# Optimization experiments

Hardware: AMD Instinct MI355X
Metric: run time of the kernel (lower is better)

## Reference

```python
import jax, jax.numpy as jnp
import numpy as np

B, T, C, H = 2, 4096, 768, 12
D = C // H  # head_dim = 64


def setup_inputs() -> dict:
    key = jax.random.key(0)
    k1, k2, k3 = jax.random.split(key, 3)
    x = jax.random.normal(k1, (B, T, C), dtype=jnp.float32)
    w_qkv = jax.random.normal(k2, (C, 3 * C), dtype=jnp.float32) * (1.0 / np.sqrt(C))
    w_out = jax.random.normal(k3, (C, C), dtype=jnp.float32) * (1.0 / np.sqrt(C))
    return {"x": x, "w_qkv": w_qkv, "w_out": w_out}


def reference(x, w_qkv, w_out):
    b, t, c = x.shape
    qkv = x @ w_qkv                              # (B,T,3C)
    q, k, v = jnp.split(qkv, 3, axis=-1)
    # (B,T,C) -> (B,H,T,D)
    q = q.reshape(b, t, H, D).transpose(0, 2, 1, 3)
    k = k.reshape(b, t, H, D).transpose(0, 2, 1, 3)
    v = v.reshape(b, t, H, D).transpose(0, 2, 1, 3)
    att = jnp.einsum('bhqd,bhkd->bhqk', q, k) / jnp.sqrt(jnp.float32(D))
    causal = jnp.tril(jnp.ones((t, t), dtype=bool))  # True where allowed
    att = jnp.where(causal, att, -jnp.inf)
    att = jax.nn.softmax(att, axis=-1)
    y = jnp.einsum('bhqk,bhkd->bhqd', att, v)        # (B,H,T,D)
    y = y.transpose(0, 2, 1, 3).reshape(b, t, c)
    return y @ w_out
```

## Files before the change

kernel.cpp:

```cpp
#include <hip/hip_runtime.h>
#include <stdint.h>
#include <stddef.h>

#define NB 2
#define NT 4096
#define NC 768
#define NH 12
#define ND 64

typedef unsigned short u16;
typedef __attribute__((ext_vector_type(4))) float f32x4;
typedef __attribute__((ext_vector_type(16))) float f32x16;
typedef __attribute__((ext_vector_type(8))) unsigned short u16x8;
typedef __attribute__((ext_vector_type(4))) unsigned short u16x4;
typedef __attribute__((ext_vector_type(8))) __bf16 bf16x8;
typedef __attribute__((ext_vector_type(4))) unsigned int u32x4;

__device__ __forceinline__ u16 f2bf(float f) {
  uint32_t u = __builtin_bit_cast(uint32_t, f);
  u += 0x7FFFu + ((u >> 16) & 1u);
  return (u16)(u >> 16);
}
__device__ __forceinline__ bf16x8 asbf(u16x8 v) { return __builtin_bit_cast(bf16x8, v); }

__device__ __forceinline__ uint32_t pkbf(float a, float b) {
  uint32_t ua = __builtin_bit_cast(uint32_t, a) + 0x8000u;
  uint32_t ub = __builtin_bit_cast(uint32_t, b) + 0x8000u;
  return __builtin_amdgcn_perm(ub, ua, 0x07060302u);
}
__device__ __forceinline__ uint32_t pktr(float a, float b) {
  return __builtin_amdgcn_perm(__builtin_bit_cast(uint32_t, b),
                               __builtin_bit_cast(uint32_t, a), 0x07060302u);
}

__global__ void k_cast(const float* __restrict__ in, u16* __restrict__ out, int n4) {
  int i = blockIdx.x * blockDim.x + threadIdx.x;
  if (i < n4) {
    f32x4 v = ((const f32x4*)in)[i];
    u16x4 o;
    o[0] = f2bf(v[0]); o[1] = f2bf(v[1]); o[2] = f2bf(v[2]); o[3] = f2bf(v[3]);
    ((u16x4*)out)[i] = o;
  }
}

__global__ void k_transpose(const float* __restrict__ in, u16* __restrict__ out,
                            int R, int Cn) {
  __shared__ float tile[32][33];
  int c0 = blockIdx.x * 32, r0 = blockIdx.y * 32;
  int tx = threadIdx.x & 31, ty = threadIdx.x >> 5;
  for (int i = ty; i < 32; i += 8)
    tile[i][tx] = in[(size_t)(r0 + i) * Cn + c0 + tx];
  __syncthreads();
  for (int i = ty; i < 32; i += 8)
    out[(size_t)(c0 + i) * R + r0 + tx] = f2bf(tile[tx][i]);
}

template <int EPI>
__global__ __launch_bounds__(256, 2)
void k_gemm_bt(const u16* __restrict__ A, const u16* __restrict__ Bt,
               int M, int N, int K,
               u16* __restrict__ o0, u16* __restrict__ o1, u16* __restrict__ o2,
               float* __restrict__ of) {
  __shared__ u16 As[128 * 40];
  __shared__ u16 Bs[128 * 40];
  const int tid = threadIdx.x;
  const int wave = tid >> 6, lane = tid & 63, quad = lane >> 4, lc = lane & 15;
  const int wm = (wave & 1) * 64, wn = (wave >> 1) * 64;
  const int bm = blockIdx.y * 128, bn = blockIdx.x * 128;

  const int sr = tid >> 2;
  const int sc8 = (tid & 3) * 8;
  const u16* ap0 = A + (size_t)(bm + sr) * K + sc8;
  const u16* ap1 = A + (size_t)(bm + 64 + sr) * K + sc8;
  const u16* bp0 = Bt + (size_t)(bn + sr) * K + sc8;
  const u16* bp1 = Bt + (size_t)(bn + 64 + sr) * K + sc8;
  u16* asl0 = &As[sr * 40 + sc8];
  u16* asl1 = &As[(64 + sr) * 40 + sc8];
  u16* bsl0 = &Bs[sr * 40 + sc8];
  u16* bsl1 = &Bs[(64 + sr) * 40 + sc8];

  f32x4 zv = {0.f, 0.f, 0.f, 0.f};
  f32x4 acc[4][4];
#pragma unroll
  for (int i = 0; i < 4; ++i)
#pragma unroll
    for (int j = 0; j < 4; ++j) acc[i][j] = zv;

  for (int k0 = 0; k0 < K; k0 += 32) {
    u16x8 a0 = *(const u16x8*)(ap0 + k0);
    u16x8 a1 = *(const u16x8*)(ap1 + k0);
    u16x8 b0 = *(const u16x8*)(bp0 + k0);
    u16x8 b1 = *(const u16x8*)(bp1 + k0);
    __syncthreads();
    *(u16x8*)asl0 = a0;
    *(u16x8*)asl1 = a1;
    *(u16x8*)bsl0 = b0;
    *(u16x8*)bsl1 = b1;
    __syncthreads();

    bf16x8 af[4], bfv[4];
#pragma unroll
    for (int mi = 0; mi < 4; ++mi)
      af[mi] = asbf(*(const u16x8*)&As[(wm + mi * 16 + lc) * 40 + quad * 8]);
#pragma unroll
    for (int ni = 0; ni < 4; ++ni)
      bfv[ni] = asbf(*(const u16x8*)&Bs[(wn + ni * 16 + lc) * 40 + quad * 8]);
#pragma unroll
    for (int mi = 0; mi < 4; ++mi)
#pragma unroll
      for (int ni = 0; ni < 4; ++ni)
        acc[mi][ni] = __builtin_amdgcn_mfma_f32_16x16x32_bf16(af[mi], bfv[ni],
                                                              acc[mi][ni], 0, 0, 0);
  }

  const int mrow0 = bm + wm + quad * 4;
#pragma unroll
  for (int mi = 0; mi < 4; ++mi) {
    const int mbase = mrow0 + mi * 16;
#pragma unroll
    for (int ni = 0; ni < 4; ++ni) {
      const int n = bn + wn + ni * 16 + lc;
      if (EPI == 0) {
#pragma unroll
        for (int r = 0; r < 4; ++r)
          of[(size_t)(mbase + r) * N + n] = acc[mi][ni][r];
      } else {
        const int sect = n / NC;
        const int wn2 = n - sect * NC;
        const int h = wn2 >> 6, d = wn2 & 63;
        const int b = mbase >> 12;
        const int t = mbase & (NT - 1);
        const float sc = (sect == 0) ? 0.18033688011112042f : 1.0f;
        if (sect == 2) {
          u16x4 pk;
#pragma unroll
          for (int r = 0; r < 4; ++r) pk[r] = f2bf(acc[mi][ni][r]);
          *(u16x4*)&o2[((size_t)(b * NH + h) * ND + d) * NT + t] = pk;
        } else {
          u16* dst = (sect == 0) ? o0 : o1;
#pragma unroll
          for (int r = 0; r < 4; ++r)
            dst[((size_t)(b * NH + h) * NT + (t + r)) * ND + d] =
                f2bf(acc[mi][ni][r] * sc);
        }
      }
    }
  }
}

__device__ __forceinline__ void softpack16(const f32x16& s, int qrel, bool msk,
                                           int l5, float& sl, bf16x8* pf) {
  float e[16];
#pragma unroll
  for (int r = 0; r < 16; ++r) {
    float v = s[r];
    if (msk) {
      int tl = (r & 3) + 8 * (r >> 2) + 4 * l5;
      v = (tl > qrel) ? -1e30f : v;
    }
    e[r] = exp2f(v);
    sl += __builtin_bit_cast(float,
          __builtin_bit_cast(uint32_t, e[r]) & 0xFFFF0000u);
  }
  uint32_t wv[8];
#pragma unroll
  for (int i = 0; i < 8; ++i) wv[i] = pktr(e[2 * i], e[2 * i + 1]);
#pragma unroll
  for (int g = 0; g < 2; ++g) {
    auto r0 = __builtin_amdgcn_permlane32_swap(wv[g * 4 + 0], wv[g * 4 + 2], false, false);
    auto r1 = __builtin_amdgcn_permlane32_swap(wv[g * 4 + 1], wv[g * 4 + 3], false, false);
    u32x4 f = {r0[0], r1[0], r0[1], r1[1]};
    pf[g] = __builtin_bit_cast(bf16x8, f);
  }
}

__global__ __launch_bounds__(256, 3)
void k_attn(const u16* __restrict__ Q, const u16* __restrict__ K,
            const u16* __restrict__ Vt, u16* __restrict__ Y) {
  __shared__ u16 SM[2][64 * 64];
  __shared__ float PL[2][64];
  const int tid = threadIdx.x;
  const int lane = tid & 63, wave = tid >> 6;
  const int l5 = lane >> 5, l31 = lane & 31;
  const int qh = wave & 1, th = wave >> 1;
  const int bh = blockIdx.x % (NB * NH);
  const int qi = 63 - blockIdx.x / (NB * NH);
  const int b = bh / NH, h = bh - b * NH;
  const u16* __restrict__ Qb = Q + (size_t)bh * NT * ND;
  const u16* __restrict__ Kb = K + (size_t)bh * NT * ND;
  const u16* __restrict__ Vb = Vt + (size_t)bh * (size_t)ND * NT;

  const int qg = qi * 64 + qh * 32 + l31;

  bf16x8 bq[4];
#pragma unroll
  for (int ks = 0; ks < 4; ++ks)
    bq[ks] = asbf(*(const u16x8*)(Qb + (size_t)qg * ND + ks * 16 + l5 * 8));

  f32x16 Zv;
#pragma unroll
  for (int i = 0; i < 16; ++i) Zv[i] = 0.f;
  f32x16 o0 = Zv, o1 = Zv;
  float sl = 0.f;

  const int srow = tid >> 3, sg = tid & 7;
  const int soff = srow * 64 + ((sg ^ (srow & 7)) * 8);
  const u16* __restrict__ pK = Kb + (size_t)srow * ND + sg * 8;
  const u16* __restrict__ pV = Vb + (size_t)srow * NT + sg * 8;

  int qfro[4];
#pragma unroll
  for (int ks = 0; ks < 4; ++ks)
    qfro[ks] = (th * 32 + l31) * 64 + (((ks * 2 + l5) ^ (l31 & 7)) * 8);
  int vfro[2];
#pragma unroll
  for (int kp = 0; kp < 2; ++kp)
    vfro[kp] = l31 * 64 + ((((2 * th + kp) * 2 + l5) ^ (l31 & 7)) * 8);

  u16x8 st[4];
  st[0] = *(const u16x8*)(pK);
  st[1] = *(const u16x8*)(pK + (size_t)32 * ND);
  st[2] = *(const u16x8*)(pV);
  st[3] = *(const u16x8*)(pV + (size_t)32 * NT);

#pragma unroll 1
  for (int tau = 0; tau <= qi; ++tau) {
    __syncthreads();
    *(u16x8*)&SM[0][soff] = st[0];
    *(u16x8*)&SM[0][2048 + soff] = st[1];
    *(u16x8*)&SM[1][soff] = st[2];
    *(u16x8*)&SM[1][2048 + soff] = st[3];
    __syncthreads();

    const bool dg = (tau == qi);
    const bool act = !(dg && th > qh);
    bf16x8 p[2];
    if (act) {
      f32x16 s = Zv;
#pragma unroll
      for (int ks = 0; ks < 4; ++ks) {
        bf16x8 kf = asbf(*(const u16x8*)&SM[0][qfro[ks]]);
        s = __builtin_amdgcn_mfma_f32_32x32x16_bf16(kf, bq[ks], s, 0, 0, 0);
      }
      softpack16(s, l31, dg && (th == qh), l5, sl, p);
    }

    if (tau < qi) {
      const int tn = (tau + 1) * 64;
      st[0] = *(const u16x8*)(pK + (size_t)tn * ND);
      st[1] = *(const u16x8*)(pK + (size_t)(tn + 32) * ND);
      st[2] = *(const u16x8*)(pV + tn);
      st[3] = *(const u16x8*)(pV + (size_t)32 * NT + tn);
    }

    if (act) {
#pragma unroll
      for (int kp = 0; kp < 2; ++kp) {
        bf16x8 v0 = asbf(*(const u16x8*)&SM[1][vfro[kp]]);
        bf16x8 v1 = asbf(*(const u16x8*)&SM[1][2048 + vfro[kp]]);
        o0 = __builtin_amdgcn_mfma_f32_32x32x16_bf16(v0, p[kp], o0, 0, 0, 0);
        o1 = __builtin_amdgcn_mfma_f32_32x32x16_bf16(v1, p[kp], o1, 0, 0, 0);
      }
    }
  }

  float l = sl + __shfl_xor(sl, 32);
  __syncthreads();
  float* PK = (float*)&SM[0][0];
  if (th == 0) {
#pragma unroll
    for (int r = 0; r < 16; ++r) PK[(qh * 32 + r) * 64 + lane] = o0[r];
#pragma unroll
    for (int r = 0; r < 16; ++r) PK[(qh * 32 + 16 + r) * 64 + lane] = o1[r];
    PL[qh][lane] = l;
  }
  __syncthreads();
  if (th == 1) {
#pragma unroll
    for (int r = 0; r < 16; ++r) o0[r] += PK[(qh * 32 + r) * 64 + lane];
#pragma unroll
    for (int r = 0; r < 16; ++r) o1[r] += PK[(qh * 32 + 16 + r) * 64 + lane];
    l += PL[qh][lane];
    const float inv = 1.f / l;
    u16* yrow = Y + (size_t)(b * NT + qg) * NC + h * 64;
#pragma unroll
    for (int dh = 0; dh < 2; ++dh) {
      const f32x16& o = dh ? o1 : o0;
#pragma unroll
      for (int rq = 0; rq < 4; ++rq) {
        const int d = dh * 32 + 8 * rq + 4 * l5;
        uint2 w;
        w.x = pkbf(o[rq * 4 + 0] * inv, o[rq * 4 + 1] * inv);
        w.y = pkbf(o[rq * 4 + 2] * inv, o[rq * 4 + 3] * inv);
        *(uint2*)&yrow[d] = w;
      }
    }
  }
}

extern "C" void kernel_launch(void* const* d_in, const int* in_sizes, int n_in,
                              void* d_out, int out_size, void* d_ws, size_t ws_size,
                              hipStream_t stream) {
  (void)in_sizes; (void)n_in; (void)out_size; (void)ws_size;
  const float* x = (const float*)d_in[0];
  const float* w_qkv = (const float*)d_in[1];
  const float* w_out = (const float*)d_in[2];
  float* out = (float*)d_out;

  u16* ws = (u16*)d_ws;
  const size_t XE = (size_t)NB * NT * NC;
  u16* xb  = ws;
  u16* wqT = xb + XE;
  u16* woT = wqT + (size_t)3 * NC * NC;
  u16* Qb  = woT + (size_t)NC * NC;
  u16* Kb  = Qb + XE;
  u16* Vtb = Kb + XE;
  u16* yb  = Vtb + XE;

  k_cast<<<(int)(XE / 4 / 256), 256, 0, stream>>>(x, xb, (int)(XE / 4));
  k_transpose<<<dim3(3 * NC / 32, NC / 32), 256, 0, stream>>>(w_qkv, wqT, NC, 3 * NC);
  k_transpose<<<dim3(NC / 32, NC / 32), 256, 0, stream>>>(w_out, woT, NC, NC);
  k_gemm_bt<1><<<dim3(3 * NC / 128, NB * NT / 128), 256, 0, stream>>>(
      xb, wqT, NB * NT, 3 * NC, NC, Qb, Kb, Vtb, nullptr);
  k_attn<<<dim3((NB * NH) * 64), 256, 0, stream>>>(Qb, Kb, Vtb, yb);
  k_gemm_bt<0><<<dim3(NC / 128, NB * NT / 128), 256, 0, stream>>>(
      yb, woT, NB * NT, NC, NC, nullptr, nullptr, nullptr, out);
}
```

Before: 246.8 us.

## Double query tile per block, double-buffer K/V via direct global-to-LDS loads

The attention kernel now handles a 128-query tile per block, so each wave holds two 32-row query fragments that share every loaded K/V tile. K and V are streamed into double-buffered LDS with global_load_lds, replacing the register staging and the two syncthreads per step with waitcnt and raw barriers. Blocks are remapped with a permuted tile order to balance causal work, and the diagonal masking is specialised through a template. This cuts LDS staging traffic and barrier count per FLOP, at the cost of more accumulator registers and more LDS per block, which could lower occupancy.

```diff
diff --git a/kernel.cpp b/kernel.cpp
--- a/kernel.cpp
+++ b/kernel.cpp
@@ -15,6 +15,9 @@
 typedef __attribute__((ext_vector_type(4))) unsigned short u16x4;
 typedef __attribute__((ext_vector_type(8))) __bf16 bf16x8;
 typedef __attribute__((ext_vector_type(4))) unsigned int u32x4;
+
+typedef __attribute__((address_space(1))) const unsigned int gu32;
+typedef __attribute__((address_space(3))) unsigned int lu32;
 
 __device__ __forceinline__ u16 f2bf(float f) {
   uint32_t u = __builtin_bit_cast(uint32_t, f);
@@ -148,15 +151,17 @@
   }
 }
 
-__device__ __forceinline__ void softpack16(const f32x16& s, int qrel, bool msk,
-                                           int l5, float& sl, bf16x8* pf) {
+
+template <bool MSK>
+__device__ __forceinline__ void softpackT(const f32x16& s, int l31, int l5,
+                                          float& sl, bf16x8* pf) {
   float e[16];
 #pragma unroll
   for (int r = 0; r < 16; ++r) {
     float v = s[r];
-    if (msk) {
+    if (MSK) {
       int tl = (r & 3) + 8 * (r >> 2) + 4 * l5;
-      v = (tl > qrel) ? -1e30f : v;
+      v = (tl > l31) ? -1e30f : v;
     }
     e[r] = exp2f(v);
     sl += __builtin_bit_cast(float,
@@ -174,39 +179,54 @@
   }
 }
 
+#define GLDS(gsrc, ldst) __builtin_amdgcn_global_load_lds( \
+    (gu32*)(gsrc), (lu32*)(ldst), 16, 0, 0)
+
 __global__ __launch_bounds__(256, 3)
 void k_attn(const u16* __restrict__ Q, const u16* __restrict__ K,
             const u16* __restrict__ Vt, u16* __restrict__ Y) {
-  __shared__ u16 SM[2][64 * 64];
-  __shared__ float PL[2][64];
+  __shared__ u16 RAW[2 * 8192 + 768];
+  __shared__ float PLs[128];
   const int tid = threadIdx.x;
   const int lane = tid & 63, wave = tid >> 6;
   const int l5 = lane >> 5, l31 = lane & 31;
   const int qh = wave & 1, th = wave >> 1;
-  const int bh = blockIdx.x % (NB * NH);
-  const int qi = 63 - blockIdx.x / (NB * NH);
+  const int o_ = blockIdx.x;
+  const int bh = o_ >> 5;
+  const int jj = ((((o_ & 31) + bh) & 31) * 11) & 31;
   const int b = bh / NH, h = bh - b * NH;
   const u16* __restrict__ Qb = Q + (size_t)bh * NT * ND;
   const u16* __restrict__ Kb = K + (size_t)bh * NT * ND;
   const u16* __restrict__ Vb = Vt + (size_t)bh * (size_t)ND * NT;
 
-  const int qg = qi * 64 + qh * 32 + l31;
-
-  bf16x8 bq[4];
-#pragma unroll
-  for (int ks = 0; ks < 4; ++ks)
-    bq[ks] = asbf(*(const u16x8*)(Qb + (size_t)qg * ND + ks * 16 + l5 * 8));
+  const int Qb0 = jj * 128;
+  const int qu0 = 4 * jj + 2 * qh;
+  const int ntau = 2 * jj + 2;
+
+  const int qgA = Qb0 + qh * 64 + l31;
+  const int qgB = qgA + 32;
+  bf16x8 bqA[4], bqB[4];
+#pragma unroll
+  for (int ks = 0; ks < 4; ++ks) {
+    bqA[ks] = asbf(*(const u16x8*)(Qb + (size_t)qgA * ND + ks * 16 + l5 * 8));
+    bqB[ks] = asbf(*(const u16x8*)(Qb + (size_t)qgB * ND + ks * 16 + l5 * 8));
+  }
 
   f32x16 Zv;
 #pragma unroll
   for (int i = 0; i < 16; ++i) Zv[i] = 0.f;
-  f32x16 o0 = Zv, o1 = Zv;
-  float sl = 0.f;
-
-  const int srow = tid >> 3, sg = tid & 7;
-  const int soff = srow * 64 + ((sg ^ (srow & 7)) * 8);
-  const u16* __restrict__ pK = Kb + (size_t)srow * ND + sg * 8;
-  const u16* __restrict__ pV = Vb + (size_t)srow * NT + sg * 8;
+  f32x16 oA0 = Zv, oA1 = Zv, oB0 = Zv, oB1 = Zv;
+  float slA = 0.f, slB = 0.f;
+
+  const int lr = lane >> 3;
+  const int gsw = ((lane & 7) ^ lr) * 8;
+  const int r0w = wave * 16;
+  const u16* gk0 = Kb + (size_t)(r0w + lr) * ND + gsw;
+  const u16* gk1 = gk0 + (size_t)8 * ND;
+  const u16* gv0 = Vb + (size_t)(r0w + lr) * NT + gsw;
+  const u16* gv1 = gv0 + (size_t)8 * NT;
+  u16* lk0 = &RAW[r0w * 64];
+  u16* lv0 = &RAW[4096 + r0w * 64];
 
   int qfro[4];
 #pragma unroll
@@ -215,84 +235,113 @@
   int vfro[2];
 #pragma unroll
   for (int kp = 0; kp < 2; ++kp)
-    vfro[kp] = l31 * 64 + ((((2 * th + kp) * 2 + l5) ^ (l31 & 7)) * 8);
-
-  u16x8 st[4];
-  st[0] = *(const u16x8*)(pK);
-  st[1] = *(const u16x8*)(pK + (size_t)32 * ND);
-  st[2] = *(const u16x8*)(pV);
-  st[3] = *(const u16x8*)(pV + (size_t)32 * NT);
+    vfro[kp] = 4096 + l31 * 64 + (((4 * th + 2 * kp + l5) ^ (l31 & 7)) * 8);
+
+  GLDS(gk0, lk0);
+  GLDS(gk1, lk0 + 512);
+  GLDS(gv0, lv0);
+  GLDS(gv1, lv0 + 512);
 
 #pragma unroll 1
-  for (int tau = 0; tau <= qi; ++tau) {
-    __syncthreads();
-    *(u16x8*)&SM[0][soff] = st[0];
-    *(u16x8*)&SM[0][2048 + soff] = st[1];
-    *(u16x8*)&SM[1][soff] = st[2];
-    *(u16x8*)&SM[1][2048 + soff] = st[3];
-    __syncthreads();
-
-    const bool dg = (tau == qi);
-    const bool act = !(dg && th > qh);
-    bf16x8 p[2];
-    if (act) {
-      f32x16 s = Zv;
+  for (int tau = 0; tau < ntau; ++tau) {
+    const int p = tau & 1;
+    if (tau + 1 < ntau) {
+      const int tn = (tau + 1) * 64;
+      const int bo = (p ^ 1) * 8192;
+      GLDS(gk0 + (size_t)tn * ND, lk0 + bo);
+      GLDS(gk1 + (size_t)tn * ND, lk0 + bo + 512);
+      GLDS(gv0 + tn, lv0 + bo);
+      GLDS(gv1 + tn, lv0 + bo + 512);
+      asm volatile("s_waitcnt vmcnt(4)" ::: "memory");
+    } else {
+      asm volatile("s_waitcnt vmcnt(0)" ::: "memory");
+    }
+    __builtin_amdgcn_s_barrier();
+
+    const int u = 2 * tau + th;
+    const int d0 = qu0 - u;
+    if (d0 >= -1) {
+      const bool act0 = (d0 >= 0);
+      const u16* bufp = &RAW[p * 8192];
+
+      f32x16 sA = Zv, sB = Zv;
 #pragma unroll
       for (int ks = 0; ks < 4; ++ks) {
-        bf16x8 kf = asbf(*(const u16x8*)&SM[0][qfro[ks]]);
-        s = __builtin_amdgcn_mfma_f32_32x32x16_bf16(kf, bq[ks], s, 0, 0, 0);
-      }
-      softpack16(s, l31, dg && (th == qh), l5, sl, p);
-    }
-
-    if (tau < qi) {
-      const int tn = (tau + 1) * 64;
-      st[0] = *(const u16x8*)(pK + (size_t)tn * ND);
-      st[1] = *(const u16x8*)(pK + (size_t)(tn + 32) * ND);
-      st[2] = *(const u16x8*)(pV + tn);
-      st[3] = *(const u16x8*)(pV + (size_t)32 * NT + tn);
-    }
-
-    if (act) {
+        bf16x8 kf = asbf(*(const u16x8*)&bufp[qfro[ks]]);
+        if (act0)
+          sA = __builtin_amdgcn_mfma_f32_32x32x16_bf16(kf, bqA[ks], sA, 0, 0, 0);
+        sB = __builtin_amdgcn_mfma_f32_32x32x16_bf16(kf, bqB[ks], sB, 0, 0, 0);
+      }
+
+      bf16x8 pA[2], pB[2];
+      if (act0) {
+        if (d0 == 0) softpackT<true>(sA, l31, l5, slA, pA);
+        else         softpackT<false>(sA, l31, l5, slA, pA);
+      }
+      if (d0 == -1) softpackT<true>(sB, l31, l5, slB, pB);
+      else          softpackT<false>(sB, l31, l5, slB, pB);
+
 #pragma unroll
       for (int kp = 0; kp < 2; ++kp) {
-        bf16x8 v0 = asbf(*(const u16x8*)&SM[1][vfro[kp]]);
-        bf16x8 v1 = asbf(*(const u16x8*)&SM[1][2048 + vfro[kp]]);
-        o0 = __builtin_amdgcn_mfma_f32_32x32x16_bf16(v0, p[kp], o0, 0, 0, 0);
-        o1 = __builtin_amdgcn_mfma_f32_32x32x16_bf16(v1, p[kp], o1, 0, 0, 0);
-      }
-    }
-  }
-
-  float l = sl + __shfl_xor(sl, 32);
+        bf16x8 v0 = asbf(*(const u16x8*)&bufp[vfro[kp]]);
+        bf16x8 v1 = asbf(*(const u16x8*)&bufp[vfro[kp] + 2048]);
+        if (act0) {
+          oA0 = __builtin_amdgcn_mfma_f32_32x32x16_bf16(v0, pA[kp], oA0, 0, 0, 0);
+          oA1 = __builtin_amdgcn_mfma_f32_32x32x16_bf16(v1, pA[kp], oA1, 0, 0, 0);
+        }
+        oB0 = __builtin_amdgcn_mfma_f32_32x32x16_bf16(v0, pB[kp], oB0, 0, 0, 0);
+        oB1 = __builtin_amdgcn_mfma_f32_32x32x16_bf16(v1, pB[kp], oB1, 0, 0, 0);
+      }
+    }
+    __builtin_amdgcn_s_barrier();
+  }
+
+  float slA2 = slA + __shfl_xor(slA, 32);
+  float slB2 = slB + __shfl_xor(slB, 32);
   __syncthreads();
-  float* PK = (float*)&SM[0][0];
+  float* PK = (float*)RAW;
   if (th == 0) {
 #pragma unroll
-    for (int r = 0; r < 16; ++r) PK[(qh * 32 + r) * 64 + lane] = o0[r];
-#pragma unroll
-    for (int r = 0; r < 16; ++r) PK[(qh * 32 + 16 + r) * 64 + lane] = o1[r];
-    PL[qh][lane] = l;
+    for (int r = 0; r < 16; ++r) {
+      const int d = (r & 3) + 8 * (r >> 2) + 4 * l5;
+      PK[(qh * 64 + l31) * 65 + d]           = oA0[r];
+      PK[(qh * 64 + l31) * 65 + 32 + d]      = oA1[r];
+      PK[(qh * 64 + 32 + l31) * 65 + d]      = oB0[r];
+      PK[(qh * 64 + 32 + l31) * 65 + 32 + d] = oB1[r];
+    }
+    PLs[qh * 64 + l31] = slA2;
+    PLs[qh * 64 + 32 + l31] = slB2;
   }
   __syncthreads();
   if (th == 1) {
 #pragma unroll
-    for (int r = 0; r < 16; ++r) o0[r] += PK[(qh * 32 + r) * 64 + lane];
-#pragma unroll
-    for (int r = 0; r < 16; ++r) o1[r] += PK[(qh * 32 + 16 + r) * 64 + lane];
-    l += PL[qh][lane];
-    const float inv = 1.f / l;
-    u16* yrow = Y + (size_t)(b * NT + qg) * NC + h * 64;
-#pragma unroll
-    for (int dh = 0; dh < 2; ++dh) {
-      const f32x16& o = dh ? o1 : o0;
-#pragma unroll
-      for (int rq = 0; rq < 4; ++rq) {
-        const int d = dh * 32 + 8 * rq + 4 * l5;
-        uint2 w;
-        w.x = pkbf(o[rq * 4 + 0] * inv, o[rq * 4 + 1] * inv);
-        w.y = pkbf(o[rq * 4 + 2] * inv, o[rq * 4 + 3] * inv);
-        *(uint2*)&yrow[d] = w;
+    for (int r = 0; r < 16; ++r) {
+      const int d = (r & 3) + 8 * (r >> 2) + 4 * l5;
+      oA0[r] += PK[(qh * 64 + l31) * 65 + d];
+      oA1[r] += PK[(qh * 64 + l31) * 65 + 32 + d];
+      oB0[r] += PK[(qh * 64 + 32 + l31) * 65 + d];
+      oB1[r] += PK[(qh * 64 + 32 + l31) * 65 + 32 + d];
+    }
+    const float invA = 1.f / (slA2 + PLs[qh * 64 + l31]);
+    const float invB = 1.f / (slB2 + PLs[qh * 64 + 32 + l31]);
+#pragma unroll
+    for (int s = 0; s < 2; ++s) {
+      const f32x16& x0 = s ? oB0 : oA0;
+      const f32x16& x1 = s ? oB1 : oA1;
+      const float inv = s ? invB : invA;
+      const int qg = s ? qgB : qgA;
+      u16* yrow = Y + (size_t)(b * NT + qg) * NC + h * 64;
+#pragma unroll
+      for (int dh = 0; dh < 2; ++dh) {
+        const f32x16& o = dh ? x1 : x0;
+#pragma unroll
+        for (int rq = 0; rq < 4; ++rq) {
+          const int d = dh * 32 + 8 * rq + 4 * l5;
+          uint2 w;
+          w.x = pkbf(o[rq * 4 + 0] * inv, o[rq * 4 + 1] * inv);
+          w.y = pkbf(o[rq * 4 + 2] * inv, o[rq * 4 + 3] * inv);
+          *(uint2*)&yrow[d] = w;
+        }
       }
     }
   }
@@ -322,7 +371,7 @@
   k_transpose<<<dim3(NC / 32, NC / 32), 256, 0, stream>>>(w_out, woT, NC, NC);
   k_gemm_bt<1><<<dim3(3 * NC / 128, NB * NT / 128), 256, 0, stream>>>(
       xb, wqT, NB * NT, 3 * NC, NC, Qb, Kb, Vtb, nullptr);
-  k_attn<<<dim3((NB * NH) * 64), 256, 0, stream>>>(Qb, Kb, Vtb, yb);
+  k_attn<<<dim3(768), 256, 0, stream>>>(Qb, Kb, Vtb, yb);
   k_gemm_bt<0><<<dim3(NC / 128, NB * NT / 128), 256, 0, stream>>>(
       yb, woT, NB * NT, NC, NC, nullptr, nullptr, nullptr, out);
 }
```

Measured after the change: 289.1 us. 17.1% more time.

## Restructure attention to single-wave blocks reading K/V directly from global memory

Applied to the files above, without the earlier changes.

The attention kernel changes from 256-thread blocks that stage K and V tiles through shared memory with barriers to single-wave blocks. Each wave owns both 32-row query halves and loads K/V fragments straight from global (L2-cached) memory. Masking is specialized through templates, and MFMA sections are bracketed with setprio to favour matrix issue. This removes LDS staging and __syncthreads overhead. In exchange each wave issues more global loads with no cross-wave reuse, and there is less explicit prefetch to hide latency.

```diff
diff --git a/kernel.cpp b/kernel.cpp
--- a/kernel.cpp
+++ b/kernel.cpp
@@ -148,15 +148,17 @@
   }
 }
 
-__device__ __forceinline__ void softpack16(const f32x16& s, int qrel, bool msk,
-                                           int l5, float& sl, bf16x8* pf) {
+
+template <bool MSK>
+__device__ __forceinline__ void softpackT(const f32x16& s, int l31, int l5,
+                                          float& sl, bf16x8* pf) {
   float e[16];
 #pragma unroll
   for (int r = 0; r < 16; ++r) {
     float v = s[r];
-    if (msk) {
+    if (MSK) {
       int tl = (r & 3) + 8 * (r >> 2) + 4 * l5;
-      v = (tl > qrel) ? -1e30f : v;
+      v = (tl > l31) ? -1e30f : v;
     }
     e[r] = exp2f(v);
     sl += __builtin_bit_cast(float,
@@ -174,15 +176,61 @@
   }
 }
 
-__global__ __launch_bounds__(256, 3)
+template <bool MA, bool MB, bool AA>
+__device__ __forceinline__ void tstep(
+    const u16* __restrict__ Kt, const u16* __restrict__ Vc,
+    int l31, int l5,
+    const bf16x8* bqA, const bf16x8* bqB,
+    f32x16& oA0, f32x16& oA1, f32x16& oB0, f32x16& oB1,
+    float& slA, float& slB, const f32x16& Zv)
+{
+  const u16* krow = Kt + (size_t)l31 * ND + l5 * 8;
+  f32x16 sA = Zv, sB = Zv;
+  __builtin_amdgcn_s_setprio(1);
+#pragma unroll
+  for (int ks = 0; ks < 4; ++ks) {
+    bf16x8 kf = asbf(*(const u16x8*)(krow + ks * 16));
+    if (AA)
+      sA = __builtin_amdgcn_mfma_f32_32x32x16_bf16(kf, bqA[ks], sA, 0, 0, 0);
+    sB = __builtin_amdgcn_mfma_f32_32x32x16_bf16(kf, bqB[ks], sB, 0, 0, 0);
+  }
+  __builtin_amdgcn_s_setprio(0);
+
+  const u16* vcol0 = Vc + l5 * 8;
+  bf16x8 v00 = asbf(*(const u16x8*)(vcol0 + (size_t)l31 * NT));
+  bf16x8 v01 = asbf(*(const u16x8*)(vcol0 + (size_t)(32 + l31) * NT));
+
+  bf16x8 pA[2], pB[2];
+  if (AA) softpackT<MA>(sA, l31, l5, slA, pA);
+  softpackT<MB>(sB, l31, l5, slB, pB);
+
+  __builtin_amdgcn_s_setprio(1);
+  if (AA) {
+    oA0 = __builtin_amdgcn_mfma_f32_32x32x16_bf16(v00, pA[0], oA0, 0, 0, 0);
+    oA1 = __builtin_amdgcn_mfma_f32_32x32x16_bf16(v01, pA[0], oA1, 0, 0, 0);
+  }
+  oB0 = __builtin_amdgcn_mfma_f32_32x32x16_bf16(v00, pB[0], oB0, 0, 0, 0);
+  oB1 = __builtin_amdgcn_mfma_f32_32x32x16_bf16(v01, pB[0], oB1, 0, 0, 0);
+  __builtin_amdgcn_s_setprio(0);
+
+  const u16* vcol1 = vcol0 + 16;
+  bf16x8 v10 = asbf(*(const u16x8*)(vcol1 + (size_t)l31 * NT));
+  bf16x8 v11 = asbf(*(const u16x8*)(vcol1 + (size_t)(32 + l31) * NT));
+  __builtin_amdgcn_s_setprio(1);
+  if (AA) {
+    oA0 = __builtin_amdgcn_mfma_f32_32x32x16_bf16(v10, pA[1], oA0, 0, 0, 0);
+    oA1 = __builtin_amdgcn_mfma_f32_32x32x16_bf16(v11, pA[1], oA1, 0, 0, 0);
+  }
+  oB0 = __builtin_amdgcn_mfma_f32_32x32x16_bf16(v10, pB[1], oB0, 0, 0, 0);
+  oB1 = __builtin_amdgcn_mfma_f32_32x32x16_bf16(v11, pB[1], oB1, 0, 0, 0);
+  __builtin_amdgcn_s_setprio(0);
+}
+
+__global__ __launch_bounds__(64, 3)
 void k_attn(const u16* __restrict__ Q, const u16* __restrict__ K,
             const u16* __restrict__ Vt, u16* __restrict__ Y) {
-  __shared__ u16 SM[2][64 * 64];
-  __shared__ float PL[2][64];
-  const int tid = threadIdx.x;
-  const int lane = tid & 63, wave = tid >> 6;
+  const int lane = threadIdx.x;
   const int l5 = lane >> 5, l31 = lane & 31;
-  const int qh = wave & 1, th = wave >> 1;
   const int bh = blockIdx.x % (NB * NH);
   const int qi = 63 - blockIdx.x / (NB * NH);
   const int b = bh / NH, h = bh - b * NH;
@@ -190,102 +238,53 @@
   const u16* __restrict__ Kb = K + (size_t)bh * NT * ND;
   const u16* __restrict__ Vb = Vt + (size_t)bh * (size_t)ND * NT;
 
-  const int qg = qi * 64 + qh * 32 + l31;
-
-  bf16x8 bq[4];
-#pragma unroll
-  for (int ks = 0; ks < 4; ++ks)
-    bq[ks] = asbf(*(const u16x8*)(Qb + (size_t)qg * ND + ks * 16 + l5 * 8));
+  const int qgA = qi * 64 + l31;
+  const int qgB = qgA + 32;
+
+  bf16x8 bqA[4], bqB[4];
+#pragma unroll
+  for (int ks = 0; ks < 4; ++ks) {
+    bqA[ks] = asbf(*(const u16x8*)(Qb + (size_t)qgA * ND + ks * 16 + l5 * 8));
+    bqB[ks] = asbf(*(const u16x8*)(Qb + (size_t)qgB * ND + ks * 16 + l5 * 8));
+  }
 
   f32x16 Zv;
 #pragma unroll
   for (int i = 0; i < 16; ++i) Zv[i] = 0.f;
-  f32x16 o0 = Zv, o1 = Zv;
-  float sl = 0.f;
-
-  const int srow = tid >> 3, sg = tid & 7;
-  const int soff = srow * 64 + ((sg ^ (srow & 7)) * 8);
-  const u16* __restrict__ pK = Kb + (size_t)srow * ND + sg * 8;
-  const u16* __restrict__ pV = Vb + (size_t)srow * NT + sg * 8;
-
-  int qfro[4];
-#pragma unroll
-  for (int ks = 0; ks < 4; ++ks)
-    qfro[ks] = (th * 32 + l31) * 64 + (((ks * 2 + l5) ^ (l31 & 7)) * 8);
-  int vfro[2];
-#pragma unroll
-  for (int kp = 0; kp < 2; ++kp)
-    vfro[kp] = l31 * 64 + ((((2 * th + kp) * 2 + l5) ^ (l31 & 7)) * 8);
-
-  u16x8 st[4];
-  st[0] = *(const u16x8*)(pK);
-  st[1] = *(const u16x8*)(pK + (size_t)32 * ND);
-  st[2] = *(const u16x8*)(pV);
-  st[3] = *(const u16x8*)(pV + (size_t)32 * NT);
+  f32x16 oA0 = Zv, oA1 = Zv, oB0 = Zv, oB1 = Zv;
+  float slA = 0.f, slB = 0.f;
 
 #pragma unroll 1
-  for (int tau = 0; tau <= qi; ++tau) {
-    __syncthreads();
-    *(u16x8*)&SM[0][soff] = st[0];
-    *(u16x8*)&SM[0][2048 + soff] = st[1];
-    *(u16x8*)&SM[1][soff] = st[2];
-    *(u16x8*)&SM[1][2048 + soff] = st[3];
-    __syncthreads();
-
-    const bool dg = (tau == qi);
-    const bool act = !(dg && th > qh);
-    bf16x8 p[2];
-    if (act) {
-      f32x16 s = Zv;
-#pragma unroll
-      for (int ks = 0; ks < 4; ++ks) {
-        bf16x8 kf = asbf(*(const u16x8*)&SM[0][qfro[ks]]);
-        s = __builtin_amdgcn_mfma_f32_32x32x16_bf16(kf, bq[ks], s, 0, 0, 0);
-      }
-      softpack16(s, l31, dg && (th == qh), l5, sl, p);
-    }
-
-    if (tau < qi) {
-      const int tn = (tau + 1) * 64;
-      st[0] = *(const u16x8*)(pK + (size_t)tn * ND);
-      st[1] = *(const u16x8*)(pK + (size_t)(tn + 32) * ND);
-      st[2] = *(const u16x8*)(pV + tn);
-      st[3] = *(const u16x8*)(pV + (size_t)32 * NT + tn);
-    }
-
-    if (act) {
-#pragma unroll
-      for (int kp = 0; kp < 2; ++kp) {
-        bf16x8 v0 = asbf(*(const u16x8*)&SM[1][vfro[kp]]);
-        bf16x8 v1 = asbf(*(const u16x8*)&SM[1][2048 + vfro[kp]]);
-        o0 = __builtin_amdgcn_mfma_f32_32x32x16_bf16(v0, p[kp], o0, 0, 0, 0);
-        o1 = __builtin_amdgcn_mfma_f32_32x32x16_bf16(v1, p[kp], o1, 0, 0, 0);
-      }
-    }
-  }
-
-  float l = sl + __shfl_xor(sl, 32);
-  __syncthreads();
-  float* PK = (float*)&SM[0][0];
-  if (th == 0) {
-#pragma unroll
-    for (int r = 0; r < 16; ++r) PK[(qh * 32 + r) * 64 + lane] = o0[r];
-#pragma unroll
-    for (int r = 0; r < 16; ++r) PK[(qh * 32 + 16 + r) * 64 + lane] = o1[r];
-    PL[qh][lane] = l;
-  }
-  __syncthreads();
-  if (th == 1) {
-#pragma unroll
-    for (int r = 0; r < 16; ++r) o0[r] += PK[(qh * 32 + r) * 64 + lane];
-#pragma unroll
-    for (int r = 0; r < 16; ++r) o1[r] += PK[(qh * 32 + 16 + r) * 64 + lane];
-    l += PL[qh][lane];
-    const float inv = 1.f / l;
+  for (int tau = 0; tau < qi; ++tau) {
+    const u16* Kt = Kb + (size_t)tau * 64 * ND;
+    const u16* Vc = Vb + tau * 64;
+    tstep<false, false, true>(Kt, Vc, l31, l5, bqA, bqB,
+                              oA0, oA1, oB0, oB1, slA, slB, Zv);
+    tstep<false, false, true>(Kt + (size_t)32 * ND, Vc + 32, l31, l5, bqA, bqB,
+                              oA0, oA1, oB0, oB1, slA, slB, Zv);
+  }
+  {
+    const u16* Kt = Kb + (size_t)qi * 64 * ND;
+    const u16* Vc = Vb + qi * 64;
+    tstep<true, false, true>(Kt, Vc, l31, l5, bqA, bqB,
+                             oA0, oA1, oB0, oB1, slA, slB, Zv);
+    tstep<false, true, false>(Kt + (size_t)32 * ND, Vc + 32, l31, l5, bqA, bqB,
+                              oA0, oA1, oB0, oB1, slA, slB, Zv);
+  }
+
+  const float lA = slA + __shfl_xor(slA, 32);
+  const float lB = slB + __shfl_xor(slB, 32);
+  const float invA = 1.f / lA, invB = 1.f / lB;
+#pragma unroll
+  for (int s = 0; s < 2; ++s) {
+    const f32x16& x0 = s ? oB0 : oA0;
+    const f32x16& x1 = s ? oB1 : oA1;
+    const float inv = s ? invB : invA;
+    const int qg = s ? qgB : qgA;
     u16* yrow = Y + (size_t)(b * NT + qg) * NC + h * 64;
 #pragma unroll
     for (int dh = 0; dh < 2; ++dh) {
-      const f32x16& o = dh ? o1 : o0;
+      const f32x16& o = dh ? x1 : x0;
 #pragma unroll
       for (int rq = 0; rq < 4; ++rq) {
         const int d = dh * 32 + 8 * rq + 4 * l5;
@@ -322,7 +321,7 @@
   k_transpose<<<dim3(NC / 32, NC / 32), 256, 0, stream>>>(w_out, woT, NC, NC);
   k_gemm_bt<1><<<dim3(3 * NC / 128, NB * NT / 128), 256, 0, stream>>>(
       xb, wqT, NB * NT, 3 * NC, NC, Qb, Kb, Vtb, nullptr);
-  k_attn<<<dim3((NB * NH) * 64), 256, 0, stream>>>(Qb, Kb, Vtb, yb);
+  k_attn<<<dim3(1536), 64, 0, stream>>>(Qb, Kb, Vtb, yb);
   k_gemm_bt<0><<<dim3(NC / 128, NB * NT / 128), 256, 0, stream>>>(
       yb, woT, NB * NT, NC, NC, nullptr, nullptr, nullptr, out);
 }
```

Measured after the change: 357.2 us. 44.7% more time.
